# Kernel optimization log

Measured on AMD Instinct MI355X. Metric: run time of the kernel, lower is better.

The kernel has to match this reference:

```python
import jax, jax.numpy as jnp
import numpy as np

B, N, C_IN, C_Z, H = 1, 2048, 128, 16, 4
C = C_IN // H  # 32 per-head dim
QB, WL, WR = 32, 48, 80  # AF3 local atom attention: 32-query blocks, 128-key window


def _ln(x, eps=1e-5):
    m = jnp.mean(x, axis=-1, keepdims=True)
    v = jnp.mean((x - m) ** 2, axis=-1, keepdims=True)
    return (x - m) * jax.lax.rsqrt(v + eps)


def setup_inputs() -> dict:
    key = jax.random.key(0)
    ks = iter(jax.random.split(key, 32))
    def rn(shape, scale=0.02):
        return jax.random.normal(next(ks), shape, jnp.float32) * scale
    d = {}
    d['single_act'] = jax.random.normal(next(ks), (B, N, C_IN), jnp.float32)
    d['pair_act'] = jax.random.normal(next(ks), (B, N, N, C_Z), jnp.float32)
    d['single_cond'] = jax.random.normal(next(ks), (B, N, C_IN), jnp.float32)
    qi = jnp.arange(N)[:, None]
    kj = jnp.arange(N)[None, :]
    blk = (qi // QB) * QB
    d['block_mask'] = (kj >= blk - WL) & (kj < blk + WR)
    # AdaptiveLayerNorm params for q and k branches
    for p in ('q', 'k'):
        d[f'lns_{p}'] = jnp.ones((C_IN,), jnp.float32)       # LN(cond) scale (no bias)
        d[f'Wgate_{p}'] = rn((C_IN, C_IN))
        d[f'bgate_{p}'] = jnp.zeros((C_IN,), jnp.float32)
        d[f'Wskip_{p}'] = rn((C_IN, C_IN))
    d['lnz_w'] = jnp.ones((C_Z,), jnp.float32)               # layer_norm_z weight (bias=False)
    d['Wq'] = rn((C_IN, C_IN)); d['bq'] = jnp.zeros((C_IN,), jnp.float32)
    d['Wk'] = rn((C_IN, C_IN))
    d['Wv'] = rn((C_IN, C_IN))
    d['Wg'] = rn((C_IN, C_IN))
    d['Wb'] = rn((C_Z, H))
    # AdaptiveZeroInit: gated output projection, gate bias init -2
    d['Wo'] = rn((C_IN, C_IN))
    d['Wgs'] = rn((C_IN, C_IN))
    d['bgs'] = jnp.full((C_IN,), -2.0, jnp.float32)
    return d


def reference(single_act, pair_act, single_cond, block_mask,
              lns_q, Wgate_q, bgate_q, Wskip_q,
              lns_k, Wgate_k, bgate_k, Wskip_k,
              lnz_w, Wq, bq, Wk, Wv, Wg, Wb, Wo, Wgs, bgs):
    def adaln(x, s, lnsw, Wgt, bgt, Wsk):
        xn = _ln(x)                 # LN without affine
        sn = _ln(s) * lnsw          # LN with scale, no bias
        return jax.nn.sigmoid(sn @ Wgt + bgt) * xn + sn @ Wsk

    a_q = adaln(single_act, single_cond, lns_q, Wgate_q, bgate_q, Wskip_q)
    a_k = adaln(single_act, single_cond, lns_k, Wgate_k, bgate_k, Wskip_k)
    z = _ln(pair_act) * lnz_w                     # [B,N,N,Cz]

    q = (a_q @ Wq + bq).reshape(B, N, H, C)
    k = (a_k @ Wk).reshape(B, N, H, C)
    v = (a_k @ Wv).reshape(B, N, H, C)
    g = (a_q @ Wg).reshape(B, N, H, C)
    bias = z @ Wb                                 # [B,N,N,H]

    scores = jnp.einsum('bihc,bjhc->bhij', q, k) * (1.0 / np.sqrt(C).astype(np.float32))
    scores = scores + jnp.transpose(bias, (0, 3, 1, 2))
    scores = jnp.where(block_mask[None, None], scores, jnp.float32(-1e9))
    attn = jax.nn.softmax(scores, axis=-1)
    o = jnp.einsum('bhij,bjhc->bihc', attn, v)    # [B,N,H,C]
    o = (jax.nn.sigmoid(g) * o).reshape(B, N, C_IN)
    # AdaptiveZeroInit: sigmoid(Linear(cond)) * LinearNoBias(o)
    return jax.nn.sigmoid(single_cond @ Wgs + bgs) * (o @ Wo)
```

## Files before the change

### kernel.cpp

```cpp
#include <hip/hip_runtime.h>
#include <hip/hip_bf16.h>

#define NTOK 2048

typedef __attribute__((ext_vector_type(8))) short short8_t;
typedef __attribute__((ext_vector_type(4))) float f32x4;

__device__ __forceinline__ float bu2f(unsigned short u) {
  unsigned int x = ((unsigned int)u) << 16; float f; __builtin_memcpy(&f, &x, 4); return f;
}
__device__ __forceinline__ unsigned short f2bu(float f) {
  __hip_bfloat16 h = __float2bfloat16(f);
  unsigned short u; __builtin_memcpy(&u, &h, 2); return u;
}
__device__ __forceinline__ float sigm(float x) { return 1.0f / (1.0f + __expf(-x)); }
__device__ __forceinline__ uint4 pack8(const float* v) {
  unsigned short u[8];
#pragma unroll
  for (int i = 0; i < 8; ++i) u[i] = f2bu(v[i]);
  uint4 r; __builtin_memcpy(&r, u, 16); return r;
}
__device__ __forceinline__ short8_t pk8s(const float* v) {
  unsigned short u[8];
#pragma unroll
  for (int i = 0; i < 8; ++i) u[i] = f2bu(v[i]);
  short8_t r; __builtin_memcpy(&r, u, 16); return r;
}

__device__ __forceinline__ short8_t wfrag(const float* __restrict__ W,
                                          const float* __restrict__ lns,
                                          int ko, int n) {
  float v[8];
#pragma unroll
  for (int i = 0; i < 8; ++i) v[i] = W[(size_t)(ko + i) * 128 + n];
  if (lns) {
    float4 l0 = *(const float4*)(lns + ko);
    float4 l1 = *(const float4*)(lns + ko + 4);
    v[0] *= l0.x; v[1] *= l0.y; v[2] *= l0.z; v[3] *= l0.w;
    v[4] *= l1.x; v[5] *= l1.y; v[6] *= l1.z; v[7] *= l1.w;
  }
  return pk8s(v);
}

__device__ __forceinline__ void gemm_dw(const unsigned short* a_lds,
                                        const float* __restrict__ W,
                                        const float* __restrict__ lns,
                                        int lm, int kg, int wv, f32x4 acc[2][2]) {
  const int xa = (lm & 7) << 3;
#pragma unroll
  for (int ks = 0; ks < 4; ++ks) {
    const int ko = ks * 32 + kg * 8;
    short8_t av[2], bv[2];
#pragma unroll
    for (int mi = 0; mi < 2; ++mi)
      av[mi] = *(const short8_t*)&a_lds[(mi * 16 + lm) * 128 + (ko ^ xa)];
#pragma unroll
    for (int ni = 0; ni < 2; ++ni)
      bv[ni] = wfrag(W, lns, ko, (wv * 2 + ni) * 16 + lm);
#pragma unroll
    for (int mi = 0; mi < 2; ++mi)
#pragma unroll
      for (int ni = 0; ni < 2; ++ni)
        acc[mi][ni] = __builtin_amdgcn_mfma_f32_16x16x32_bf16(av[mi], bv[ni], acc[mi][ni], 0, 0, 0);
  }
}

__global__ __launch_bounds__(256) void bias_proj_kernel(
    const float* __restrict__ act, const float* __restrict__ cond,
    const float* __restrict__ lns_q, const float* __restrict__ lns_k,
    const float* __restrict__ WgQ, const float* __restrict__ WsQ,
    const float* __restrict__ WgK, const float* __restrict__ WsK,
    const float* __restrict__ Wq, const float* __restrict__ Wk,
    const float* __restrict__ Wv, const float* __restrict__ Wg,
    const float* __restrict__ Wgs,
    const float* __restrict__ bgate_q, const float* __restrict__ bgate_k,
    const float* __restrict__ bq, const float* __restrict__ bgs,
    const float* __restrict__ pair, const float* __restrict__ lnz_w,
    const float* __restrict__ Wb,
    unsigned short* __restrict__ q_b, unsigned short* __restrict__ k_b,
    unsigned short* __restrict__ vt_b, unsigned short* __restrict__ gsig_b,
    unsigned short* __restrict__ gs_b, unsigned short* __restrict__ bias_h)
{
  __shared__ unsigned short a_lds[32 * 128];
  __shared__ unsigned short xn_lds[32 * 136];
  __shared__ unsigned short a2_lds[32 * 128];
  __shared__ float lw[16];
  __shared__ float wbz[16][4];
  const int tid = threadIdx.x;
  const int bid = blockIdx.x;

  if (bid >= 320) {
    if (tid < 16) lw[tid] = lnz_w[tid];
    if (tid < 64) wbz[tid >> 2][tid & 3] = Wb[tid];
    __syncthreads();
    const int idx = (bid - 320) * 256 + tid;
    const int i = idx >> 7, jw = idx & 127;
    const int j = ((i >> 5) << 5) - 48 + jw;
    float bo[4] = {-1e9f, -1e9f, -1e9f, -1e9f};
    if (j >= 0 && j < NTOK) {
      const float4* p = (const float4*)(pair + ((size_t)i * NTOK + j) * 16);
      float4 z0 = p[0], z1 = p[1], z2 = p[2], z3 = p[3];
      float z[16] = {z0.x, z0.y, z0.z, z0.w, z1.x, z1.y, z1.z, z1.w,
                     z2.x, z2.y, z2.z, z2.w, z3.x, z3.y, z3.z, z3.w};
      float s = 0.f, ss = 0.f;
#pragma unroll
      for (int c = 0; c < 16; ++c) { s += z[c]; ss += z[c]*z[c]; }
      const float m = s * (1.f/16.f), v = ss * (1.f/16.f) - m*m;
      const float r = rsqrtf(v + 1e-5f);
      bo[0] = bo[1] = bo[2] = bo[3] = 0.f;
#pragma unroll
      for (int c = 0; c < 16; ++c) {
        const float zn = (z[c] - m) * r * lw[c];
        bo[0] += zn * wbz[c][0]; bo[1] += zn * wbz[c][1];
        bo[2] += zn * wbz[c][2]; bo[3] += zn * wbz[c][3];
      }
    }
#pragma unroll
    for (int h = 0; h < 4; ++h)
      bias_h[(size_t)h * (NTOK * 128) + idx] = f2bu(bo[h]);
    return;
  }

  const int br = bid / 64;
  const int rt = bid % 64;
  const int row0 = rt * 32;
  const int l = tid & 63, wv = tid >> 6;
  const int lm = l & 15, kg = l >> 4;

  {
    const int r = tid >> 3;
    const int c0 = (tid & 7) << 4;
    float xv[16], cv[16];
    const float4* ap = (const float4*)(act + (size_t)(row0 + r) * 128 + c0);
    const float4* cp = (const float4*)(cond + (size_t)(row0 + r) * 128 + c0);
#pragma unroll
    for (int i = 0; i < 4; ++i) {
      float4 a4 = ap[i], b4 = cp[i];
      xv[4*i+0]=a4.x; xv[4*i+1]=a4.y; xv[4*i+2]=a4.z; xv[4*i+3]=a4.w;
      cv[4*i+0]=b4.x; cv[4*i+1]=b4.y; cv[4*i+2]=b4.z; cv[4*i+3]=b4.w;
    }
    float sx=0.f, sxx=0.f, sc=0.f, scc=0.f;
#pragma unroll
    for (int i = 0; i < 16; ++i) { sx+=xv[i]; sxx+=xv[i]*xv[i]; sc+=cv[i]; scc+=cv[i]*cv[i]; }
#pragma unroll
    for (int m = 1; m < 8; m <<= 1) {
      sx += __shfl_xor(sx, m); sxx += __shfl_xor(sxx, m);
      sc += __shfl_xor(sc, m); scc += __shfl_xor(scc, m);
    }
    const float mx = sx * (1.f/128.f), vx = sxx*(1.f/128.f) - mx*mx;
    const float mc = sc * (1.f/128.f), vc = scc*(1.f/128.f) - mc*mc;
    const float rx = rsqrtf(vx + 1e-5f), rc = rsqrtf(vc + 1e-5f);
    float xo[16], so[16];
#pragma unroll
    for (int i = 0; i < 16; ++i) { xo[i] = (xv[i]-mx)*rx; so[i] = (cv[i]-mc)*rc; }
    const int x = (r & 7) << 3;
    if (br == 4) {
      *(uint4*)&a_lds[r * 128 + (c0 ^ x)] = pack8(cv);
      *(uint4*)&a_lds[r * 128 + ((c0 + 8) ^ x)] = pack8(cv + 8);
    } else {
      *(uint4*)&a_lds[r * 128 + (c0 ^ x)] = pack8(so);
      *(uint4*)&a_lds[r * 128 + ((c0 + 8) ^ x)] = pack8(so + 8);
      *(uint4*)&xn_lds[r * 136 + c0] = pack8(xo);
      *(uint4*)&xn_lds[r * 136 + c0 + 8] = pack8(xo + 8);
    }
  }
  __syncthreads();

  if (br == 4) {
    f32x4 acc[2][2] = {};
    gemm_dw(a_lds, Wgs, nullptr, lm, kg, wv, acc);
    float bgv[2];
#pragma unroll
    for (int ni = 0; ni < 2; ++ni) bgv[ni] = bgs[(wv * 2 + ni) * 16 + lm];
#pragma unroll
    for (int mi = 0; mi < 2; ++mi)
#pragma unroll
      for (int ni = 0; ni < 2; ++ni)
#pragma unroll
        for (int r = 0; r < 4; ++r) {
          const int rl = mi * 16 + kg * 4 + r;
          const int n = (wv * 2 + ni) * 16 + lm;
          gs_b[(size_t)(row0 + rl) * 128 + n] = f2bu(sigm(acc[mi][ni][r] + bgv[ni]));
        }
    return;
  }

  const bool useq = (br < 2);
  const float* Wgt = useq ? WgQ : WgK;
  const float* Wsk = useq ? WsQ : WsK;
  const float* lns = useq ? lns_q : lns_k;
  const float* bg  = useq ? bgate_q : bgate_k;

  f32x4 ag[2][2] = {}, as2[2][2] = {};
  gemm_dw(a_lds, Wgt, lns, lm, kg, wv, ag);
  gemm_dw(a_lds, Wsk, lns, lm, kg, wv, as2);
  {
    float bgv[2];
#pragma unroll
    for (int ni = 0; ni < 2; ++ni) bgv[ni] = bg[(wv * 2 + ni) * 16 + lm];
#pragma unroll
    for (int mi = 0; mi < 2; ++mi)
#pragma unroll
      for (int ni = 0; ni < 2; ++ni)
#pragma unroll
        for (int r = 0; r < 4; ++r) {
          const int rl = mi * 16 + kg * 4 + r;
          const int n = (wv * 2 + ni) * 16 + lm;
          const float gate = sigm(ag[mi][ni][r] + bgv[ni]);
          const float a = gate * bu2f(xn_lds[rl * 136 + n]) + as2[mi][ni][r];
          a2_lds[rl * 128 + (n ^ ((rl & 7) << 3))] = f2bu(a);
        }
  }
  __syncthreads();

  const float* Wout = (br == 0) ? Wq : (br == 1) ? Wg : (br == 2) ? Wk : Wv;
  f32x4 ao[2][2] = {};
  gemm_dw(a2_lds, Wout, nullptr, lm, kg, wv, ao);

  if (br == 3) {
#pragma unroll
    for (int mi = 0; mi < 2; ++mi)
#pragma unroll
      for (int ni = 0; ni < 2; ++ni) {
        const int n = (wv * 2 + ni) * 16 + lm;
        const int tok0 = row0 + mi * 16 + kg * 4;
        ushort4 o;
        o.x = f2bu(ao[mi][ni][0]); o.y = f2bu(ao[mi][ni][1]);
        o.z = f2bu(ao[mi][ni][2]); o.w = f2bu(ao[mi][ni][3]);
        *(ushort4*)(vt_b + (size_t)n * NTOK + tok0) = o;
      }
    return;
  }
  const float scale = 0.17677669529663687f;
  float bqv[2] = {0.f, 0.f};
  if (br == 0) {
#pragma unroll
    for (int ni = 0; ni < 2; ++ni) bqv[ni] = bq[(wv * 2 + ni) * 16 + lm];
  }
  unsigned short* dst = (br == 0) ? q_b : (br == 1) ? gsig_b : k_b;
#pragma unroll
  for (int mi = 0; mi < 2; ++mi)
#pragma unroll
    for (int ni = 0; ni < 2; ++ni)
#pragma unroll
      for (int r = 0; r < 4; ++r) {
        const int rl = mi * 16 + kg * 4 + r;
        const int n = (wv * 2 + ni) * 16 + lm;
        float v = ao[mi][ni][r];
        if (br == 0) v = (v + bqv[ni]) * scale;
        else if (br == 1) v = sigm(v);
        dst[(size_t)(row0 + rl) * 128 + n] = f2bu(v);
      }
}

__global__ __launch_bounds__(256) void attn_kernel(
    const unsigned short* __restrict__ q_b, const unsigned short* __restrict__ k_b,
    const unsigned short* __restrict__ vt_b, const unsigned short* __restrict__ gsig_b,
    const unsigned short* __restrict__ bias_h, unsigned short* __restrict__ o_b)
{
  __shared__ unsigned short k_lds[128 * 64];
  __shared__ unsigned short vt[32 * 128];
  __shared__ unsigned short p_lds[32 * 128];
  __shared__ unsigned short q_lds[32 * 64];
  __shared__ unsigned short bias_lds[32 * 136];
  __shared__ float mxlds[4][32];
  __shared__ float smlds[4][32];
  __shared__ f32x4 op[16][64];
  const int tid = threadIdx.x;
  const int h = blockIdx.x & 3, b = blockIdx.x >> 2;
  const int j0 = b * 32 - 48;
  const int l = tid & 63, wv = tid >> 6;
  const int lm = l & 15, kg = l >> 4;

  {
    const int r = tid >> 3, c0 = (tid & 7) << 2;
    ushort4 v = *(const ushort4*)(q_b + (size_t)(b * 32 + r) * 128 + h * 32 + c0);
    *(ushort4*)&q_lds[r * 64 + (c0 ^ ((r & 7) << 3))] = v;
  }
  {
    const int r = tid >> 3, c0 = (tid & 7) << 4;
    const uint4* g = (const uint4*)(bias_h + (size_t)h * (NTOK * 128) + (size_t)(b * 32 + r) * 128 + c0);
    uint4 v0 = g[0], v1 = g[1];
    *(uint4*)&bias_lds[r * 136 + c0] = v0;
    *(uint4*)&bias_lds[r * 136 + c0 + 8] = v1;
  }
  {
    const int jw = tid >> 1, cb = (tid & 1) << 4;
    const int j = j0 + jw;
    uint4 kv0 = {0,0,0,0}, kv1 = {0,0,0,0};
    if (j >= 0 && j < NTOK) {
      const uint4* gk = (const uint4*)(k_b + (size_t)j * 128 + h * 32 + cb);
      kv0 = gk[0]; kv1 = gk[1];
    }
    const int xk = (jw & 7) << 3;
    *(uint4*)&k_lds[jw * 64 + (cb ^ xk)] = kv0;
    *(uint4*)&k_lds[jw * 64 + ((cb + 8) ^ xk)] = kv1;
  }
  {
    const int c = tid >> 3, koff = (tid & 7) << 4;
    const int j = j0 + koff;
    uint4 v0 = {0,0,0,0}, v1 = {0,0,0,0};
    if (j >= 0 && j + 15 < NTOK) {
      const uint4* gv = (const uint4*)(vt_b + (size_t)(h * 32 + c) * NTOK + j);
      v0 = gv[0]; v1 = gv[1];
    }
    const int xc = (c & 7) << 3;
    *(uint4*)&vt[c * 128 + (koff ^ xc)] = v0;
    *(uint4*)&vt[c * 128 + ((koff + 8) ^ xc)] = v1;
  }
  __syncthreads();

  f32x4 sc[2][2] = {};
  {
    const int xa = (lm & 7) << 3;
    short8_t aq[2], bk[2];
#pragma unroll
    for (int mi = 0; mi < 2; ++mi)
      aq[mi] = *(const short8_t*)&q_lds[(mi * 16 + lm) * 64 + ((kg * 8) ^ xa)];
#pragma unroll
    for (int ni = 0; ni < 2; ++ni) {
      const int key = (wv * 2 + ni) * 16 + lm;
      bk[ni] = *(const short8_t*)&k_lds[key * 64 + ((kg * 8) ^ ((key & 7) << 3))];
    }
#pragma unroll
    for (int mi = 0; mi < 2; ++mi)
#pragma unroll
      for (int ni = 0; ni < 2; ++ni)
        sc[mi][ni] = __builtin_amdgcn_mfma_f32_16x16x32_bf16(aq[mi], bk[ni], sc[mi][ni], 0, 0, 0);
  }
  float sv[2][2][4];
#pragma unroll
  for (int mi = 0; mi < 2; ++mi)
#pragma unroll
    for (int ni = 0; ni < 2; ++ni)
#pragma unroll
      for (int r = 0; r < 4; ++r) {
        const int q = mi * 16 + kg * 4 + r;
        const int key = (wv * 2 + ni) * 16 + lm;
        sv[mi][ni][r] = sc[mi][ni][r] + bu2f(bias_lds[q * 136 + key]);
      }
#pragma unroll
  for (int mi = 0; mi < 2; ++mi)
#pragma unroll
    for (int r = 0; r < 4; ++r) {
      float m0 = fmaxf(sv[mi][0][r], sv[mi][1][r]);
#pragma unroll
      for (int msk = 1; msk < 16; msk <<= 1) m0 = fmaxf(m0, __shfl_xor(m0, msk));
      if (lm == 0) mxlds[wv][mi * 16 + kg * 4 + r] = m0;
    }
  __syncthreads();
#pragma unroll
  for (int mi = 0; mi < 2; ++mi)
#pragma unroll
    for (int r = 0; r < 4; ++r) {
      const int q = mi * 16 + kg * 4 + r;
      const float m = fmaxf(fmaxf(mxlds[0][q], mxlds[1][q]), fmaxf(mxlds[2][q], mxlds[3][q]));
      float s = 0.f;
#pragma unroll
      for (int ni = 0; ni < 2; ++ni) {
        const float e = __expf(sv[mi][ni][r] - m);
        const int key = (wv * 2 + ni) * 16 + lm;
        p_lds[q * 128 + ((key & 7) | ((key & 120) ^ ((q & 7) << 3)))] = f2bu(e);
        s += e;
      }
#pragma unroll
      for (int msk = 1; msk < 16; msk <<= 1) s += __shfl_xor(s, msk);
      if (lm == 0) smlds[wv][q] = s;
    }
  f32x4 oacc[2][2] = {};
  {
    const int key0 = wv * 32 + kg * 8;
    short8_t pa[2], vbf[2];
#pragma unroll
    for (int mi = 0; mi < 2; ++mi) {
      const int q = mi * 16 + lm;
      pa[mi] = *(const short8_t*)&p_lds[q * 128 + (key0 ^ ((q & 7) << 3))];
    }
#pragma unroll
    for (int ct = 0; ct < 2; ++ct) {
      const int c = ct * 16 + lm;
      vbf[ct] = *(const short8_t*)&vt[c * 128 + (key0 ^ ((c & 7) << 3))];
    }
#pragma unroll
    for (int mi = 0; mi < 2; ++mi)
#pragma unroll
      for (int ct = 0; ct < 2; ++ct)
        oacc[mi][ct] = __builtin_amdgcn_mfma_f32_16x16x32_bf16(pa[mi], vbf[ct], oacc[mi][ct], 0, 0, 0);
  }
#pragma unroll
  for (int mi = 0; mi < 2; ++mi)
#pragma unroll
    for (int ct = 0; ct < 2; ++ct)
      op[wv * 4 + mi * 2 + ct][l] = oacc[mi][ct];
  __syncthreads();
  {
    const int q = tid >> 3, c0 = (tid & 7) << 2;
    const int mt = q >> 4, g = (q >> 2) & 3, r = q & 3;
    const float tot = smlds[0][q] + smlds[1][q] + smlds[2][q] + smlds[3][q];
    const float inv = 1.f / tot;
    ushort4 gg = *(const ushort4*)(gsig_b + (size_t)(b * 32 + q) * 128 + h * 32 + c0);
    unsigned short gga[4] = {gg.x, gg.y, gg.z, gg.w};
    unsigned short outa[4];
#pragma unroll
    for (int i2 = 0; i2 < 4; ++i2) {
      const int c = c0 + i2;
      const int ct = c >> 4, lane = g * 16 + (c & 15);
      float s = 0.f;
#pragma unroll
      for (int w2 = 0; w2 < 4; ++w2)
        s += ((const float*)&op[w2 * 4 + mt * 2 + ct][lane])[r];
      outa[i2] = f2bu(s * inv * bu2f(gga[i2]));
    }
    ushort4 ov; ov.x = outa[0]; ov.y = outa[1]; ov.z = outa[2]; ov.w = outa[3];
    *(ushort4*)(o_b + (size_t)(b * 32 + q) * 128 + h * 32 + c0) = ov;
  }
}

__global__ __launch_bounds__(256) void out_kernel(
    const float* __restrict__ Wo, const unsigned short* __restrict__ o_b,
    const unsigned short* __restrict__ gs_b, float* __restrict__ out)
{
  __shared__ unsigned short a_lds[16 * 128];
  const int tid = threadIdx.x;
  const int row0 = blockIdx.x * 16;
  const int l = tid & 63, wv = tid >> 6;
  const int lm = l & 15, kg = l >> 4;
  {
    const int r = tid >> 4, c0 = (tid & 15) << 3;
    uint4 v = *(const uint4*)(o_b + (size_t)(row0 + r) * 128 + c0);
    *(uint4*)&a_lds[r * 128 + (c0 ^ ((r & 7) << 3))] = v;
  }
  __syncthreads();
  f32x4 acc[2] = {};
  const int xa = (lm & 7) << 3;
#pragma unroll
  for (int ks = 0; ks < 4; ++ks) {
    const int ko = ks * 32 + kg * 8;
    short8_t av = *(const short8_t*)&a_lds[lm * 128 + (ko ^ xa)];
#pragma unroll
    for (int ni = 0; ni < 2; ++ni) {
      short8_t bv = wfrag(Wo, nullptr, ko, (wv * 2 + ni) * 16 + lm);
      acc[ni] = __builtin_amdgcn_mfma_f32_16x16x32_bf16(av, bv, acc[ni], 0, 0, 0);
    }
  }
#pragma unroll
  for (int ni = 0; ni < 2; ++ni)
#pragma unroll
    for (int r = 0; r < 4; ++r) {
      const int rl = kg * 4 + r;
      const int n = (wv * 2 + ni) * 16 + lm;
      const float gsv = bu2f(gs_b[(size_t)(row0 + rl) * 128 + n]);
      out[(size_t)(row0 + rl) * 128 + n] = acc[ni][r] * gsv;
    }
}

extern "C" void kernel_launch(void* const* d_in, const int* in_sizes, int n_in,
                              void* d_out, int out_size, void* d_ws, size_t ws_size,
                              hipStream_t stream) {
  const float* act     = (const float*)d_in[0];
  const float* pair    = (const float*)d_in[1];
  const float* cond    = (const float*)d_in[2];
  const float* lns_q   = (const float*)d_in[4];
  const float* Wgate_q = (const float*)d_in[5];
  const float* bgate_q = (const float*)d_in[6];
  const float* Wskip_q = (const float*)d_in[7];
  const float* lns_k   = (const float*)d_in[8];
  const float* Wgate_k = (const float*)d_in[9];
  const float* bgate_k = (const float*)d_in[10];
  const float* Wskip_k = (const float*)d_in[11];
  const float* lnz_w   = (const float*)d_in[12];
  const float* Wq      = (const float*)d_in[13];
  const float* bq      = (const float*)d_in[14];
  const float* Wk      = (const float*)d_in[15];
  const float* Wv      = (const float*)d_in[16];
  const float* Wg      = (const float*)d_in[17];
  const float* Wb      = (const float*)d_in[18];
  const float* Wo      = (const float*)d_in[19];
  const float* Wgs     = (const float*)d_in[20];
  const float* bgs     = (const float*)d_in[21];
  float* out           = (float*)d_out;

  unsigned short* ws = (unsigned short*)d_ws;
  unsigned short* q_b    = ws;
  unsigned short* k_b    = ws + 262144;
  unsigned short* vt_b   = ws + 524288;
  unsigned short* gsig_b = ws + 786432;
  unsigned short* gs_b   = ws + 1048576;
  unsigned short* o_b    = ws + 1310720;
  unsigned short* bias_h = ws + 1572864;

  hipLaunchKernelGGL(bias_proj_kernel, dim3(1344), dim3(256), 0, stream,
                     act, cond, lns_q, lns_k,
                     Wgate_q, Wskip_q, Wgate_k, Wskip_k,
                     Wq, Wk, Wv, Wg, Wgs,
                     bgate_q, bgate_k, bq, bgs,
                     pair, lnz_w, Wb,
                     q_b, k_b, vt_b, gsig_b, gs_b, bias_h);
  hipLaunchKernelGGL(attn_kernel, dim3(256), dim3(256), 0, stream,
                     q_b, k_b, vt_b, gsig_b, bias_h, o_b);
  hipLaunchKernelGGL(out_kernel, dim3(128), dim3(256), 0, stream,
                     Wo, o_b, gs_b, out);
}
```

Before: 25.91 us.

## Split bias and projection kernels; restructure PV matmul to per-wave output tiles

The combined bias/projection kernel becomes two separate launches, so the bias-only blocks no longer reserve the projection kernel's LDS footprint. In the attention kernel, the PV product now gives each wave its own 16x16 output tile over the full 128-key reduction. This replaces the split-K partial sums that went through a large LDS buffer and a cross-wave reduction, dropping that buffer and one reduction pass. The cost is an extra kernel launch, plus narrower scalar stores for gating and output where ushort4 vector stores were used before.

```diff
diff --git a/kernel.cpp b/kernel.cpp
--- a/kernel.cpp
+++ b/kernel.cpp
@@ -65,7 +65,44 @@
   }
 }
 
-__global__ __launch_bounds__(256) void bias_proj_kernel(
+__global__ __launch_bounds__(256) void bias_kernel(
+    const float* __restrict__ pair, const float* __restrict__ lnz_w,
+    const float* __restrict__ Wb, unsigned short* __restrict__ bias_h)
+{
+  __shared__ float lw[16];
+  __shared__ float wbz[16][4];
+  const int tid = threadIdx.x;
+  if (tid < 16) lw[tid] = lnz_w[tid];
+  if (tid < 64) wbz[tid >> 2][tid & 3] = Wb[tid];
+  __syncthreads();
+  const int idx = blockIdx.x * 256 + tid;
+  const int i = idx >> 7, jw = idx & 127;
+  const int j = ((i >> 5) << 5) - 48 + jw;
+  float bo[4] = {-1e9f, -1e9f, -1e9f, -1e9f};
+  if (j >= 0 && j < NTOK) {
+    const float4* p = (const float4*)(pair + ((size_t)i * NTOK + j) * 16);
+    float4 z0 = p[0], z1 = p[1], z2 = p[2], z3 = p[3];
+    float z[16] = {z0.x, z0.y, z0.z, z0.w, z1.x, z1.y, z1.z, z1.w,
+                   z2.x, z2.y, z2.z, z2.w, z3.x, z3.y, z3.z, z3.w};
+    float s = 0.f, ss = 0.f;
+#pragma unroll
+    for (int c = 0; c < 16; ++c) { s += z[c]; ss += z[c]*z[c]; }
+    const float m = s * (1.f/16.f), v = ss * (1.f/16.f) - m*m;
+    const float r = rsqrtf(v + 1e-5f);
+    bo[0] = bo[1] = bo[2] = bo[3] = 0.f;
+#pragma unroll
+    for (int c = 0; c < 16; ++c) {
+      const float zn = (z[c] - m) * r * lw[c];
+      bo[0] += zn * wbz[c][0]; bo[1] += zn * wbz[c][1];
+      bo[2] += zn * wbz[c][2]; bo[3] += zn * wbz[c][3];
+    }
+  }
+#pragma unroll
+  for (int h = 0; h < 4; ++h)
+    bias_h[(size_t)h * (NTOK * 128) + idx] = f2bu(bo[h]);
+}
+
+__global__ __launch_bounds__(256) void proj_kernel(
     const float* __restrict__ act, const float* __restrict__ cond,
     const float* __restrict__ lns_q, const float* __restrict__ lns_k,
     const float* __restrict__ WgQ, const float* __restrict__ WsQ,
@@ -75,54 +112,16 @@
     const float* __restrict__ Wgs,
     const float* __restrict__ bgate_q, const float* __restrict__ bgate_k,
     const float* __restrict__ bq, const float* __restrict__ bgs,
-    const float* __restrict__ pair, const float* __restrict__ lnz_w,
-    const float* __restrict__ Wb,
     unsigned short* __restrict__ q_b, unsigned short* __restrict__ k_b,
     unsigned short* __restrict__ vt_b, unsigned short* __restrict__ gsig_b,
-    unsigned short* __restrict__ gs_b, unsigned short* __restrict__ bias_h)
+    unsigned short* __restrict__ gs_b)
 {
   __shared__ unsigned short a_lds[32 * 128];
   __shared__ unsigned short xn_lds[32 * 136];
   __shared__ unsigned short a2_lds[32 * 128];
-  __shared__ float lw[16];
-  __shared__ float wbz[16][4];
   const int tid = threadIdx.x;
-  const int bid = blockIdx.x;
-
-  if (bid >= 320) {
-    if (tid < 16) lw[tid] = lnz_w[tid];
-    if (tid < 64) wbz[tid >> 2][tid & 3] = Wb[tid];
-    __syncthreads();
-    const int idx = (bid - 320) * 256 + tid;
-    const int i = idx >> 7, jw = idx & 127;
-    const int j = ((i >> 5) << 5) - 48 + jw;
-    float bo[4] = {-1e9f, -1e9f, -1e9f, -1e9f};
-    if (j >= 0 && j < NTOK) {
-      const float4* p = (const float4*)(pair + ((size_t)i * NTOK + j) * 16);
-      float4 z0 = p[0], z1 = p[1], z2 = p[2], z3 = p[3];
-      float z[16] = {z0.x, z0.y, z0.z, z0.w, z1.x, z1.y, z1.z, z1.w,
-                     z2.x, z2.y, z2.z, z2.w, z3.x, z3.y, z3.z, z3.w};
-      float s = 0.f, ss = 0.f;
-#pragma unroll
-      for (int c = 0; c < 16; ++c) { s += z[c]; ss += z[c]*z[c]; }
-      const float m = s * (1.f/16.f), v = ss * (1.f/16.f) - m*m;
-      const float r = rsqrtf(v + 1e-5f);
-      bo[0] = bo[1] = bo[2] = bo[3] = 0.f;
-#pragma unroll
-      for (int c = 0; c < 16; ++c) {
-        const float zn = (z[c] - m) * r * lw[c];
-        bo[0] += zn * wbz[c][0]; bo[1] += zn * wbz[c][1];
-        bo[2] += zn * wbz[c][2]; bo[3] += zn * wbz[c][3];
-      }
-    }
-#pragma unroll
-    for (int h = 0; h < 4; ++h)
-      bias_h[(size_t)h * (NTOK * 128) + idx] = f2bu(bo[h]);
-    return;
-  }
-
-  const int br = bid / 64;
-  const int rt = bid % 64;
+  const int br = blockIdx.x / 64;
+  const int rt = blockIdx.x % 64;
   const int row0 = rt * 32;
   const int l = tid & 63, wv = tid >> 6;
   const int lm = l & 15, kg = l >> 4;
@@ -265,7 +264,6 @@
   __shared__ unsigned short bias_lds[32 * 136];
   __shared__ float mxlds[4][32];
   __shared__ float smlds[4][32];
-  __shared__ f32x4 op[16][64];
   const int tid = threadIdx.x;
   const int h = blockIdx.x & 3, b = blockIdx.x >> 2;
   const int j0 = b * 32 - 48;
@@ -367,52 +365,30 @@
       for (int msk = 1; msk < 16; msk <<= 1) s += __shfl_xor(s, msk);
       if (lm == 0) smlds[wv][q] = s;
     }
-  f32x4 oacc[2][2] = {};
-  {
-    const int key0 = wv * 32 + kg * 8;
-    short8_t pa[2], vbf[2];
-#pragma unroll
-    for (int mi = 0; mi < 2; ++mi) {
-      const int q = mi * 16 + lm;
-      pa[mi] = *(const short8_t*)&p_lds[q * 128 + (key0 ^ ((q & 7) << 3))];
-    }
-#pragma unroll
-    for (int ct = 0; ct < 2; ++ct) {
-      const int c = ct * 16 + lm;
-      vbf[ct] = *(const short8_t*)&vt[c * 128 + (key0 ^ ((c & 7) << 3))];
-    }
-#pragma unroll
-    for (int mi = 0; mi < 2; ++mi)
-#pragma unroll
-      for (int ct = 0; ct < 2; ++ct)
-        oacc[mi][ct] = __builtin_amdgcn_mfma_f32_16x16x32_bf16(pa[mi], vbf[ct], oacc[mi][ct], 0, 0, 0);
-  }
-#pragma unroll
-  for (int mi = 0; mi < 2; ++mi)
-#pragma unroll
-    for (int ct = 0; ct < 2; ++ct)
-      op[wv * 4 + mi * 2 + ct][l] = oacc[mi][ct];
-  __syncthreads();
-  {
-    const int q = tid >> 3, c0 = (tid & 7) << 2;
-    const int mt = q >> 4, g = (q >> 2) & 3, r = q & 3;
-    const float tot = smlds[0][q] + smlds[1][q] + smlds[2][q] + smlds[3][q];
-    const float inv = 1.f / tot;
-    ushort4 gg = *(const ushort4*)(gsig_b + (size_t)(b * 32 + q) * 128 + h * 32 + c0);
-    unsigned short gga[4] = {gg.x, gg.y, gg.z, gg.w};
-    unsigned short outa[4];
-#pragma unroll
-    for (int i2 = 0; i2 < 4; ++i2) {
-      const int c = c0 + i2;
-      const int ct = c >> 4, lane = g * 16 + (c & 15);
-      float s = 0.f;
-#pragma unroll
-      for (int w2 = 0; w2 < 4; ++w2)
-        s += ((const float*)&op[w2 * 4 + mt * 2 + ct][lane])[r];
-      outa[i2] = f2bu(s * inv * bu2f(gga[i2]));
-    }
-    ushort4 ov; ov.x = outa[0]; ov.y = outa[1]; ov.z = outa[2]; ov.w = outa[3];
-    *(ushort4*)(o_b + (size_t)(b * 32 + q) * 128 + h * 32 + c0) = ov;
+  __syncthreads();
+
+  {
+    const int rh = (wv & 1) << 4, ch = (wv >> 1) << 4;
+    const int rowl = rh + lm;
+    const int coll = ch + lm;
+    const int xr = (rowl & 7) << 3, xc = (coll & 7) << 3;
+    f32x4 acc = {};
+#pragma unroll
+    for (int ks = 0; ks < 4; ++ks) {
+      const int ko = ks * 32 + kg * 8;
+      short8_t pa = *(const short8_t*)&p_lds[rowl * 128 + (ko ^ xr)];
+      short8_t vb = *(const short8_t*)&vt[coll * 128 + (ko ^ xc)];
+      acc = __builtin_amdgcn_mfma_f32_16x16x32_bf16(pa, vb, acc, 0, 0, 0);
+    }
+#pragma unroll
+    for (int r = 0; r < 4; ++r) {
+      const int row = rh + kg * 4 + r;
+      const int col = ch + lm;
+      const float tot = smlds[0][row] + smlds[1][row] + smlds[2][row] + smlds[3][row];
+      const float inv = 1.f / tot;
+      const float gsv = bu2f(gsig_b[(size_t)(b * 32 + row) * 128 + h * 32 + col]);
+      o_b[(size_t)(b * 32 + row) * 128 + h * 32 + col] = f2bu(acc[r] * inv * gsv);
+    }
   }
 }
 
@@ -489,13 +465,14 @@
   unsigned short* o_b    = ws + 1310720;
   unsigned short* bias_h = ws + 1572864;
 
-  hipLaunchKernelGGL(bias_proj_kernel, dim3(1344), dim3(256), 0, stream,
+  hipLaunchKernelGGL(bias_kernel, dim3(1024), dim3(256), 0, stream,
+                     pair, lnz_w, Wb, bias_h);
+  hipLaunchKernelGGL(proj_kernel, dim3(320), dim3(256), 0, stream,
                      act, cond, lns_q, lns_k,
                      Wgate_q, Wskip_q, Wgate_k, Wskip_k,
                      Wq, Wk, Wv, Wg, Wgs,
                      bgate_q, bgate_k, bq, bgs,
-                     pair, lnz_w, Wb,
-                     q_b, k_b, vt_b, gsig_b, gs_b, bias_h);
+                     q_b, k_b, vt_b, gsig_b, gs_b);
   hipLaunchKernelGGL(attn_kernel, dim3(256), dim3(256), 0, stream,
                      q_b, k_b, vt_b, gsig_b, bias_h, o_b);
   hipLaunchKernelGGL(out_kernel, dim3(128), dim3(256), 0, stream,
```

Result: slower. 29.55 us (+14.1%).
